# Kernel tuning notes

Measured on AMD Instinct MI355X. Metric: run time of the kernel, lower is better.

Reference implementation:

```python
import jax, jax.numpy as jnp
import numpy as np

B, N, M, D, H = 2, 2048, 2048, 1024, 16
HD = D // H          # head_dim = 64
F = int(D * 4.0)     # mlp hidden = 4096
EPS = 1e-5


def layernorm(x, w, b):
    mu = jnp.mean(x, axis=-1, keepdims=True)
    var = jnp.mean(jnp.square(x - mu), axis=-1, keepdims=True)
    return (x - mu) * jax.lax.rsqrt(var + EPS) * w + b


def setup_inputs() -> dict:
    key = jax.random.key(0)
    ks = jax.random.split(key, 8)
    w = lambda k, shape: jax.random.normal(k, shape, dtype=jnp.float32) * 0.02
    return {
        "query": jax.random.normal(ks[0], (B, N, D), dtype=jnp.float32),
        "context": jax.random.normal(ks[1], (B, M, D), dtype=jnp.float32),
        "qpos": jax.random.randint(ks[2], (B, N), 0, N, dtype=jnp.int32),
        "cpos": jax.random.randint(ks[3], (B, M), 0, M, dtype=jnp.int32),
        "Wq_w": w(ks[4], (D, D)), "Wq_b": jnp.zeros((D,), jnp.float32),
        "Wk_w": w(ks[5], (D, D)), "Wk_b": jnp.zeros((D,), jnp.float32),
        "Wv_w": w(ks[6], (D, D)), "Wv_b": jnp.zeros((D,), jnp.float32),
        "qn_w": jnp.ones((HD,), jnp.float32), "qn_b": jnp.zeros((HD,), jnp.float32),
        "kn_w": jnp.ones((HD,), jnp.float32), "kn_b": jnp.zeros((HD,), jnp.float32),
        "ffn_w": jnp.ones((D,), jnp.float32), "ffn_b": jnp.zeros((D,), jnp.float32),
        "fc1_w": w(ks[7], (D, F)), "fc1_b": jnp.zeros((F,), jnp.float32),
        "fc2_w": w(jax.random.fold_in(key, 99), (F, D)), "fc2_b": jnp.zeros((D,), jnp.float32),
    }


def reference(query, context, qpos, cpos,
              Wq_w, Wq_b, Wk_w, Wk_b, Wv_w, Wv_b,
              qn_w, qn_b, kn_w, kn_b,
              ffn_w, ffn_b, fc1_w, fc1_b, fc2_w, fc2_b):
    # rope=None -> qpos/cpos unused (kept for signature fidelity)
    res = query
    # QKV projections, split heads -> (B,H,T,HD)
    Q = (query @ Wq_w + Wq_b).reshape(B, N, H, HD).transpose(0, 2, 1, 3)
    K = (context @ Wk_w + Wk_b).reshape(B, M, H, HD).transpose(0, 2, 1, 3)
    V = (context @ Wv_w + Wv_b).reshape(B, M, H, HD).transpose(0, 2, 1, 3)
    # per-head LayerNorm on q and k
    Q = layernorm(Q, qn_w, qn_b)
    K = layernorm(K, kn_w, kn_b)
    # attention
    scores = jnp.einsum('bhnd,bhmd->bhnm', Q, K) / jnp.sqrt(jnp.float32(HD))
    attn = jax.nn.softmax(scores, axis=-1)
    out = jnp.einsum('bhnm,bhmd->bhnd', attn, V)
    out = out.transpose(0, 2, 1, 3).reshape(B, N, D)
    out = res + out
    # MLP block with pre-norm
    res2 = out
    h = layernorm(out, ffn_w, ffn_b)
    h = jax.nn.gelu(h @ fc1_w + fc1_b, approximate=False)
    h = h @ fc2_w + fc2_b
    return res2 + h
```

## Files before the change

### kernel.cpp

```cpp
#include <hip/hip_runtime.h>
#include <hip/hip_bf16.h>
#include <math.h>

constexpr int Bb  = 2;
constexpr int Nn  = 2048;
constexpr int Mm  = 2048;
constexpr int Dd  = 1024;
constexpr int Hh  = 16;
constexpr int HD  = 64;
constexpr int Ff  = 4096;
constexpr float EPS = 1e-5f;
constexpr float QSCALE = 0.125f * 1.4426950408889634f;
constexpr float SMAX = 12.0f;

typedef __attribute__((ext_vector_type(8))) short bf16x8;
typedef __attribute__((ext_vector_type(4))) short bf16x4;
typedef __attribute__((ext_vector_type(4))) float f32x4;

__device__ inline unsigned short f2bf(float f) {
    __hip_bfloat16 h = __float2bfloat16(f);
    return *reinterpret_cast<unsigned short*>(&h);
}
__device__ inline unsigned short f2bf_rh(float f) {
    union { float f; unsigned u; } c{f};
    return (unsigned short)((c.u + 0x8000u) >> 16);
}
__device__ inline float bf2f(unsigned short u) {
    union { unsigned u; float f; } c{(unsigned)u << 16};
    return c.f;
}

__device__ inline float gelu_fast(float x) {
    float t = x * x;
    float f = fmaf(-0.10295004f, t, -2.30211782f);
    float e = __builtin_amdgcn_exp2f(x * f);
    return x * __builtin_amdgcn_rcpf(1.0f + e);
}

__device__ inline void async_load16(const void* g, void* l) {
    __builtin_amdgcn_global_load_lds(
        (const __attribute__((address_space(1))) void*)g,
        (__attribute__((address_space(3))) void*)l, 16, 0, 0);
}

__global__ __launch_bounds__(256) void prep_kernel(
    const float* __restrict__ query, const float* __restrict__ context,
    unsigned short* __restrict__ qa, unsigned short* __restrict__ ca,
    const float* __restrict__ W0, const float* __restrict__ W1,
    const float* __restrict__ W2, const float* __restrict__ W3,
    const float* __restrict__ W4,
    unsigned short* __restrict__ T0, unsigned short* __restrict__ T1,
    unsigned short* __restrict__ T2, unsigned short* __restrict__ T3,
    unsigned short* __restrict__ T4)
{
    __shared__ float tile[32][33];
    int bid = blockIdx.x;
    if (bid < 8192) {
        int i = bid * 256 + threadIdx.x;
        const float* x; unsigned short* y; int k;
        if (i < 1048576) { x = query; y = qa; k = i; }
        else { x = context; y = ca; k = i - 1048576; }
        float4 v = reinterpret_cast<const float4*>(x)[k];
        ushort4 o;
        o.x = f2bf(v.x); o.y = f2bf(v.y); o.z = f2bf(v.z); o.w = f2bf(v.w);
        reinterpret_cast<ushort4*>(y)[k] = o;
        return;
    }
    bid -= 8192;
    const float* W; unsigned short* T; int K, Cn, tid;
    if (bid < 3072) {
        int j = bid >> 10; tid = bid & 1023;
        W = (j == 0) ? W0 : (j == 1) ? W1 : W2;
        T = (j == 0) ? T0 : (j == 1) ? T1 : T2;
        K = Dd; Cn = Dd;
    } else if (bid < 7168) {
        tid = bid - 3072; W = W3; T = T3; K = Dd; Cn = Ff;
    } else {
        tid = bid - 7168; W = W4; T = T4; K = Ff; Cn = Dd;
    }
    int xt = Cn >> 5;
    int bx = tid % xt, by = tid / xt;
    int tx = threadIdx.x & 31, ty = threadIdx.x >> 5;
    int c = bx * 32 + tx;
    int kbase = by * 32;
#pragma unroll
    for (int i = ty; i < 32; i += 8)
        tile[i][tx] = W[(size_t)(kbase + i) * Cn + c];
    __syncthreads();
    int k = kbase + tx;
#pragma unroll
    for (int i = ty; i < 32; i += 8)
        T[(size_t)(bx * 32 + i) * K + k] = f2bf(tile[tx][i]);
}

__global__ __launch_bounds__(256) void qkv_fused_kernel(
    const unsigned short* __restrict__ qa, const unsigned short* __restrict__ ca,
    const unsigned short* __restrict__ Wqt, const unsigned short* __restrict__ Wkt,
    const unsigned short* __restrict__ Wvt,
    const float* __restrict__ bq, const float* __restrict__ bk,
    const float* __restrict__ bv,
    const float* __restrict__ qn_w, const float* __restrict__ qn_b,
    const float* __restrict__ kn_w, const float* __restrict__ kn_b,
    unsigned short* __restrict__ Qbh, unsigned short* __restrict__ Kbh,
    unsigned short* __restrict__ Vt_g)
{
    __shared__ __align__(16) unsigned short As[2][128 * 32];
    __shared__ __align__(16) unsigned short Bs[2][128 * 32];

    const int bz = blockIdx.z;
    const unsigned short* A  = (bz == 0) ? qa : ca;
    const unsigned short* Bt = (bz == 0) ? Wqt : (bz == 1) ? Wkt : Wvt;
    const float* bias        = (bz == 0) ? bq  : (bz == 1) ? bk  : bv;
    const int K = Dd;

    const int t    = threadIdx.x;
    const int wave = t >> 6;
    const int lane = t & 63;
    const int r0 = blockIdx.y * 128;
    const int c0 = blockIdx.x * 128;
    const int wm = (wave >> 1) * 64;
    const int wn = (wave & 1) * 64;

    f32x4 acc[4][4];
#pragma unroll
    for (int i = 0; i < 4; i++)
#pragma unroll
        for (int j = 0; j < 4; j++) acc[i][j] = (f32x4)0.0f;

    const int row1 = t >> 2;
    const int kcs  = ((t & 3) ^ ((t >> 3) & 3)) * 8;
    const size_t arow1 = (size_t)(r0 + row1) * K + kcs;
    const size_t arow2 = (size_t)(r0 + row1 + 64) * K + kcs;
    const size_t brow1 = (size_t)(c0 + row1) * K + kcs;
    const size_t brow2 = (size_t)(c0 + row1 + 64) * K + kcs;
    char* A1_0 = (char*)&As[0][0] + wave * 1024;
    char* A2_0 = (char*)&As[0][0] + 4096 + wave * 1024;
    char* B1_0 = (char*)&Bs[0][0] + wave * 1024;
    char* B2_0 = (char*)&Bs[0][0] + 4096 + wave * 1024;
    char* A1_1 = (char*)&As[1][0] + wave * 1024;
    char* A2_1 = (char*)&As[1][0] + 4096 + wave * 1024;
    char* B1_1 = (char*)&Bs[1][0] + wave * 1024;
    char* B2_1 = (char*)&Bs[1][0] + 4096 + wave * 1024;

    const int m   = lane & 15;
    const int swc = ((lane >> 4) ^ ((m >> 1) & 3)) << 3;

    async_load16(A + arow1, A1_0);
    async_load16(A + arow2, A2_0);
    async_load16(Bt + brow1, B1_0);
    async_load16(Bt + brow2, B2_0);

    for (int k0 = 0; k0 < K; k0 += 32) {
        __syncthreads();
        const int cur = (k0 >> 5) & 1;
        if (k0 + 32 < K) {
            const int nk = k0 + 32;
            async_load16(A + arow1 + nk, cur ? A1_0 : A1_1);
            async_load16(A + arow2 + nk, cur ? A2_0 : A2_1);
            async_load16(Bt + brow1 + nk, cur ? B1_0 : B1_1);
            async_load16(Bt + brow2 + nk, cur ? B2_0 : B2_1);
        }
        const unsigned short* Ac = &As[cur][0];
        const unsigned short* Bc = &Bs[cur][0];

        bf16x8 af[4], bfr[4];
#pragma unroll
        for (int mi = 0; mi < 4; mi++)
            af[mi] = *(const bf16x8*)&Ac[(wm + mi * 16 + m) * 32 + swc];
#pragma unroll
        for (int nj = 0; nj < 4; nj++)
            bfr[nj] = *(const bf16x8*)&Bc[(wn + nj * 16 + m) * 32 + swc];
#pragma unroll
        for (int mi = 0; mi < 4; mi++)
#pragma unroll
            for (int nj = 0; nj < 4; nj++)
                acc[mi][nj] = __builtin_amdgcn_mfma_f32_16x16x32_bf16(
                    af[mi], bfr[nj], acc[mi][nj], 0, 0, 0);
    }

    const int rowb = r0 + wm + (lane >> 4) * 4;
    const int colb = c0 + wn + m;
#pragma unroll
    for (int nj = 0; nj < 4; nj++) {
        float bvv = bias[colb + nj * 16];
#pragma unroll
        for (int mi = 0; mi < 4; mi++)
#pragma unroll
            for (int r = 0; r < 4; r++) acc[mi][nj][r] += bvv;
    }

    if (bz < 2) {
        unsigned short* O = (bz == 0) ? Qbh : Kbh;
        const float* lw = (bz == 0) ? qn_w : kn_w;
        const float* lb = (bz == 0) ? qn_b : kn_b;
        const float scale = (bz == 0) ? QSCALE : 1.0f;
        const int hcol = c0 + wn;
        float w4[4], b4[4];
#pragma unroll
        for (int nj = 0; nj < 4; nj++) {
            int d = nj * 16 + m;
            w4[nj] = lw[d]; b4[nj] = lb[d];
        }
#pragma unroll
        for (int mi = 0; mi < 4; mi++) {
#pragma unroll
            for (int r = 0; r < 4; r++) {
                float s = (acc[mi][0][r] + acc[mi][1][r]) +
                          (acc[mi][2][r] + acc[mi][3][r]);
                s += __shfl_xor(s, 1); s += __shfl_xor(s, 2);
                s += __shfl_xor(s, 4); s += __shfl_xor(s, 8);
                float mu = s * (1.0f / 64.0f);
                float v2 = 0.f;
#pragma unroll
                for (int nj = 0; nj < 4; nj++) {
                    float dd = acc[mi][nj][r] - mu; v2 += dd * dd;
                }
                v2 += __shfl_xor(v2, 1); v2 += __shfl_xor(v2, 2);
                v2 += __shfl_xor(v2, 4); v2 += __shfl_xor(v2, 8);
                float rstd = rsqrtf(v2 * (1.0f / 64.0f) + EPS);
                size_t base = (size_t)(rowb + mi * 16 + r) * Dd + hcol;
#pragma unroll
                for (int nj = 0; nj < 4; nj++) {
                    int d = nj * 16 + m;
                    O[base + d] = f2bf(
                        ((acc[mi][nj][r] - mu) * rstd * w4[nj] + b4[nj]) * scale);
                }
            }
        }
    } else {
#pragma unroll
        for (int mi = 0; mi < 4; mi++) {
            int row0 = rowb + mi * 16;
            int bidx = row0 >> 11;
            int mtok = row0 & (Mm - 1);
#pragma unroll
            for (int nj = 0; nj < 4; nj++) {
                int col = colb + nj * 16;
                int h = col >> 6, d = col & 63;
                ushort4 o;
                o.x = f2bf(acc[mi][nj][0]);
                o.y = f2bf(acc[mi][nj][1]);
                o.z = f2bf(acc[mi][nj][2]);
                o.w = f2bf(acc[mi][nj][3]);
                *(ushort4*)(Vt_g + (((size_t)(bidx * Hh + h) * HD + d) << 11) + mtok) = o;
            }
        }
    }
}

#define QUAD(MH, BB, NH)                                                      \
    {                                                                         \
        _Pragma("unroll")                                                     \
        for (int miq = 0; miq < 4; ++miq) {                                   \
            _Pragma("unroll")                                                 \
            for (int njq = 0; njq < 2; ++njq) {                               \
                _Pragma("unroll")                                             \
                for (int ks = 0; ks < 2; ++ks) {                              \
                    acc[(MH) * 4 + miq][(NH) * 2 + njq] =                     \
                        __builtin_amdgcn_mfma_f32_16x16x32_bf16(              \
                            afr[miq][ks], BB[njq][ks],                        \
                            acc[(MH) * 4 + miq][(NH) * 2 + njq], 0, 0, 0);    \
                }                                                             \
            }                                                                 \
        }                                                                     \
    }

template <int MODE>
__global__ __launch_bounds__(512, 2) void gemm_8ph(
    const unsigned short* __restrict__ A,
    const unsigned short* __restrict__ Bt,
    const float* __restrict__ bias,
    unsigned short* __restrict__ Out)
{
    extern __shared__ char smem[];

    constexpr int KstC = (MODE == 0) ? Dd : Ff;
    constexpr int CnC  = (MODE == 0) ? Ff : Dd;
    constexpr int NI   = 16;

    const int chunk  = blockIdx.x & 7;
    const int within = blockIdx.x >> 3;
    int r0, c0, koff = 0;
    if (MODE == 0) {
        const int bx = (chunk & 3) * 4 + (within & 3);
        const int by = (chunk >> 2) * 8 + (within >> 2);
        r0 = by * 256; c0 = bx * 256;
    } else {
        const int split = chunk >> 1;
        const int bx = within & 3;
        const int by = (chunk & 1) * 8 + (within >> 2);
        r0 = by * 256; c0 = bx * 256; koff = split * (Ff / 4);
        Out += (size_t)split * ((size_t)Bb * Nn * Dd);
    }

    const int t    = threadIdx.x;
    const int wave = t >> 6;
    const int lane = t & 63;
    const int m16  = lane & 15;
    const int kg4  = lane >> 4;
    const int wr   = wave >> 2;
    const int wc   = wave & 3;

    const int u  = t >> 3;
    const int cl = ((t & 7) ^ (u & 7)) * 8;
    const unsigned short* sA0 = A + (size_t)(r0 + u) * KstC + koff + cl;
    const unsigned short* sA1 = A + (size_t)(r0 + 128 + u) * KstC + koff + cl;
    const int rB = (u & 31) + ((u >> 5) << 6);
    const unsigned short* sB0 = Bt + (size_t)(c0 + rB) * KstC + koff + cl;
    const unsigned short* sB1 = Bt + (size_t)(c0 + 128 + rB) * KstC + koff + cl;

    int rdA[4], rdB[2], ck[2];
#pragma unroll
    for (int miq = 0; miq < 4; miq++) rdA[miq] = (wr * 64 + miq * 16 + m16) * 128;
#pragma unroll
    for (int njq = 0; njq < 2; njq++) rdB[njq] = (wc * 32 + njq * 16 + m16) * 128;
#pragma unroll
    for (int ks = 0; ks < 2; ks++) ck[ks] = (((ks * 4 + kg4) ^ (m16 & 7)) << 4);

    f32x4 acc[8][4];
#pragma unroll
    for (int i = 0; i < 8; i++)
#pragma unroll
        for (int j = 0; j < 4; j++) acc[i][j] = (f32x4)0.0f;

    bf16x8 afr[4][2], b0r[2][2], b1r[2][2];

    auto stA = [&](int mh, int nd, int kel) {
        char* d = smem + nd * 65536 + mh * 16384 + wave * 1024;
        async_load16(sA0 + (size_t)mh * 64 * KstC + kel, d);
        async_load16(sA1 + (size_t)mh * 64 * KstC + kel, d + 8192);
    };
    auto stB = [&](int nh, int nd, int kel) {
        char* d = smem + nd * 65536 + 32768 + nh * 16384 + wave * 1024;
        async_load16(sB0 + (size_t)nh * 32 * KstC + kel, d);
        async_load16(sB1 + (size_t)nh * 32 * KstC + kel, d + 8192);
    };
    auto ldA = [&](int cd, int mh) {
        const char* base = smem + cd * 65536 + mh * 16384;
#pragma unroll
        for (int miq = 0; miq < 4; miq++)
#pragma unroll
            for (int ks = 0; ks < 2; ks++)
                afr[miq][ks] = *(const bf16x8*)(base + rdA[miq] + ck[ks]);
    };
    auto ldB = [&](int cd, int nh, bf16x8 (&bb)[2][2]) {
        const char* base = smem + cd * 65536 + 32768 + nh * 16384;
#pragma unroll
        for (int njq = 0; njq < 2; njq++)
#pragma unroll
            for (int ks = 0; ks < 2; ks++)
                bb[njq][ks] = *(const bf16x8*)(base + rdB[njq] + ck[ks]);
    };

    stA(0, 0, 0); stB(0, 0, 0); stB(1, 0, 0); stA(1, 0, 0);
    asm volatile("s_waitcnt vmcnt(0)" ::: "memory");
    asm volatile("s_barrier" ::: "memory");

    for (int it = 0; it < NI - 1; ++it) {
        const int cd = it & 1, nd = cd ^ 1;
        const int kn = (it + 1) * 64;
        ldA(cd, 0); ldB(cd, 0, b0r);
        stA(0, nd, kn);
        asm volatile("s_waitcnt vmcnt(4)" ::: "memory");
        asm volatile("s_barrier" ::: "memory");
        QUAD(0, b0r, 0)
        ldB(cd, 1, b1r);
        stB(0, nd, kn);
        asm volatile("s_waitcnt vmcnt(4)" ::: "memory");
        asm volatile("s_barrier" ::: "memory");
        QUAD(0, b1r, 1)
        ldA(cd, 1);
        stB(1, nd, kn);
        asm volatile("s_barrier" ::: "memory");
        QUAD(1, b1r, 1)
        stA(1, nd, kn);
        asm volatile("s_waitcnt vmcnt(4)" ::: "memory");
        asm volatile("s_barrier" ::: "memory");
        QUAD(1, b0r, 0)
    }

    {
        const int cd = (NI - 1) & 1;
        ldA(cd, 0); ldB(cd, 0, b0r);
        asm volatile("s_waitcnt vmcnt(2)" ::: "memory");
        asm volatile("s_barrier" ::: "memory");
        QUAD(0, b0r, 0)
        ldB(cd, 1, b1r);
        asm volatile("s_waitcnt vmcnt(0)" ::: "memory");
        asm volatile("s_barrier" ::: "memory");
        QUAD(0, b1r, 1)
        ldA(cd, 1);
        QUAD(1, b1r, 1)
        QUAD(1, b0r, 0)
    }

#pragma unroll
    for (int MI = 0; MI < 8; MI++) {
        const int row = r0 + wr * 128 + MI * 16 + kg4 * 4;
#pragma unroll
        for (int NJ = 0; NJ < 4; NJ++) {
            const int col = c0 + wc * 64 + NJ * 16 + m16;
            if (MODE == 0) {
                const float bv = bias[col];
#pragma unroll
                for (int rr = 0; rr < 4; rr++) {
                    float v = acc[MI][NJ][rr] + bv;
                    v = gelu_fast(v);
                    Out[(size_t)(row + rr) * CnC + col] = f2bf(v);
                }
            } else {
#pragma unroll
                for (int rr = 0; rr < 4; rr++)
                    Out[(size_t)(row + rr) * CnC + col] = f2bf(acc[MI][NJ][rr]);
            }
        }
    }
}

__global__ __launch_bounds__(512) void attention_mfma_kernel(
    const unsigned short* __restrict__ Qb,
    const unsigned short* __restrict__ Kb,
    const unsigned short* __restrict__ Vt_g,
    const float* __restrict__ query,
    float* __restrict__ Out);

namespace {
struct GemmAttrInit {
    GemmAttrInit() {
        hipFuncSetAttribute(reinterpret_cast<const void*>(&gemm_8ph<0>),
                            hipFuncAttributeMaxDynamicSharedMemorySize, 131072);
        hipFuncSetAttribute(reinterpret_cast<const void*>(&gemm_8ph<1>),
                            hipFuncAttributeMaxDynamicSharedMemorySize, 131072);
        hipFuncSetAttribute(reinterpret_cast<const void*>(&attention_mfma_kernel),
                            hipFuncAttributeMaxDynamicSharedMemorySize, 69632);
    }
};
GemmAttrInit g_gemm_attr_init;
}

__global__ __launch_bounds__(256) void fc2_reduce_kernel(
    const unsigned short* __restrict__ Part, const float* __restrict__ bias,
    const float* __restrict__ attn, float* __restrict__ out)
{
    constexpr size_t NEl = (size_t)Bb * Nn * Dd;
    size_t i4 = (size_t)blockIdx.x * 256 + threadIdx.x;
    size_t i = i4 * 4;
    float4 s = *reinterpret_cast<const float4*>(attn + i);
    float4 bv = *reinterpret_cast<const float4*>(bias + (i & (Dd - 1)));
    s.x += bv.x; s.y += bv.y; s.z += bv.z; s.w += bv.w;
#pragma unroll
    for (int sp = 0; sp < 4; sp++) {
        ushort4 u = *reinterpret_cast<const ushort4*>(Part + sp * NEl + i);
        s.x += bf2f(u.x); s.y += bf2f(u.y); s.z += bf2f(u.z); s.w += bf2f(u.w);
    }
    *reinterpret_cast<float4*>(out + i) = s;
}

__global__ __launch_bounds__(256) void ln_row_bf16_kernel(
    const float* __restrict__ X, const float* __restrict__ w,
    const float* __restrict__ b, unsigned short* __restrict__ Y)
{
    int row = blockIdx.x;
    const float* x = X + (size_t)row * Dd;
    int t = threadIdx.x;
    float v[4];
    float s = 0.f;
#pragma unroll
    for (int i = 0; i < 4; i++) { v[i] = x[t + i * 256]; s += v[i]; }
#pragma unroll
    for (int off = 32; off; off >>= 1) s += __shfl_xor(s, off);
    __shared__ float red[4];
    __shared__ float stats[2];
    if ((t & 63) == 0) red[t >> 6] = s;
    __syncthreads();
    if (t == 0) stats[0] = (red[0] + red[1] + red[2] + red[3]) * (1.0f / Dd);
    __syncthreads();
    float mu = stats[0];
    float s2 = 0.f;
#pragma unroll
    for (int i = 0; i < 4; i++) { float d = v[i] - mu; s2 += d * d; }
#pragma unroll
    for (int off = 32; off; off >>= 1) s2 += __shfl_xor(s2, off);
    __syncthreads();
    if ((t & 63) == 0) red[t >> 6] = s2;
    __syncthreads();
    if (t == 0) stats[1] = (red[0] + red[1] + red[2] + red[3]) * (1.0f / Dd);
    __syncthreads();
    float rstd = rsqrtf(stats[1] + EPS);
    unsigned short* y = Y + (size_t)row * Dd;
#pragma unroll
    for (int i = 0; i < 4; i++) {
        int c = t + i * 256;
        y[c] = f2bf((v[i] - mu) * rstd * w[c] + b[c]);
    }
}

__global__ __launch_bounds__(512) void attention_mfma_kernel(
    const unsigned short* __restrict__ Qb,
    const unsigned short* __restrict__ Kb,
    const unsigned short* __restrict__ Vt_g,
    const float* __restrict__ query,
    float* __restrict__ Out)
{
    extern __shared__ char asmem[];

    const int bid = blockIdx.x;
    const int g  = bid & 31;
    const int qt = bid >> 5;
    const int b  = g >> 4;
    const int h  = g & 15;
    const int q0 = qt * 256;

    const int t    = threadIdx.x;
    const int wave = t >> 6;
    const int lane = t & 63;
    const int m16  = lane & 15;
    const int kg   = lane >> 4;
    const int swc  = (kg ^ ((m16 >> 1) & 3)) << 3;

    bf16x8 qf[2][2];
#pragma unroll
    for (int rh = 0; rh < 2; rh++) {
        const unsigned short* qp =
            Qb + ((size_t)(b * Nn + q0 + wave * 32 + rh * 16 + m16) * Dd + h * HD + kg * 8);
        qf[rh][0] = *(const bf16x8*)qp;
        qf[rh][1] = *(const bf16x8*)(qp + 32);
    }

    f32x4 oacc[2][4];
    float lrow[2][4];
#pragma unroll
    for (int rh = 0; rh < 2; rh++)
#pragma unroll
        for (int i = 0; i < 4; i++) { oacc[rh][i] = (f32x4)0.f; lrow[rh][i] = 0.f; }

    const size_t kbase  = (size_t)(b * Mm) * Dd + h * HD;
    const size_t vtbase = ((size_t)(b * Hh + h) * HD) * Mm;
    unsigned short* psw = (unsigned short*)(asmem + 32768) + wave * (32 * 72);

    const int u    = t & 255;
    const int pan  = t >> 8;
    const int srow = u >> 2;
    const int schk = ((u & 3) ^ ((srow >> 1) & 3)) * 8;
    char* kdstA = asmem +     0 + pan * 4096 + (wave & 3) * 1024;
    char* kdstB = asmem +  8192 + pan * 4096 + (wave & 3) * 1024;
    char* vdstA = asmem + 16384 + pan * 4096 + (wave & 3) * 1024;
    char* vdstB = asmem + 24576 + pan * 4096 + (wave & 3) * 1024;
    const unsigned short* kp0 = Kb + kbase + (size_t)srow * Dd + schk + pan * 32;
    const unsigned short* vp0 = Vt_g + vtbase + (size_t)srow * Mm + schk + pan * 32;

    async_load16(kp0, kdstA);
    async_load16(vp0, vdstA);

    for (int m0 = 0; m0 < Mm; m0 += 64) {
        __syncthreads();
        const int cur = (m0 >> 6) & 1;
        if (m0 + 64 < Mm) {
            async_load16(kp0 + (size_t)(m0 + 64) * Dd, cur ? kdstA : kdstB);
            async_load16(vp0 + (m0 + 64),              cur ? vdstA : vdstB);
        }
        const unsigned short* Kc = (const unsigned short*)(asmem + cur * 8192);
        const unsigned short* Vc = (const unsigned short*)(asmem + 16384 + cur * 8192);

        f32x4 s[2][4];
#pragma unroll
        for (int j = 0; j < 4; j++) {
            bf16x8 b0 = *(const bf16x8*)&Kc[(j * 16 + m16) * 32 + swc];
            bf16x8 b1 = *(const bf16x8*)&Kc[2048 + (j * 16 + m16) * 32 + swc];
#pragma unroll
            for (int rh = 0; rh < 2; rh++) {
                f32x4 a = (f32x4)(-SMAX);
                a = __builtin_amdgcn_mfma_f32_16x16x32_bf16(qf[rh][0], b0, a, 0, 0, 0);
                a = __builtin_amdgcn_mfma_f32_16x16x32_bf16(qf[rh][1], b1, a, 0, 0, 0);
                s[rh][j] = a;
            }
        }

#pragma unroll
        for (int rh = 0; rh < 2; rh++) {
#pragma unroll
            for (int r = 0; r < 4; r++) {
                float p0 = __builtin_amdgcn_exp2f(s[rh][0][r]);
                float p1 = __builtin_amdgcn_exp2f(s[rh][1][r]);
                float p2 = __builtin_amdgcn_exp2f(s[rh][2][r]);
                float p3 = __builtin_amdgcn_exp2f(s[rh][3][r]);
                lrow[rh][r] += (p0 + p1) + (p2 + p3);
                int qrow = rh * 16 + kg * 4 + r;
                psw[qrow * 72 +  0 + m16] = f2bf_rh(p0);
                psw[qrow * 72 + 16 + m16] = f2bf_rh(p1);
                psw[qrow * 72 + 32 + m16] = f2bf_rh(p2);
                psw[qrow * 72 + 48 + m16] = f2bf_rh(p3);
            }
        }

        bf16x8 pf[2][2];
#pragma unroll
        for (int rh = 0; rh < 2; rh++) {
            pf[rh][0] = *(const bf16x8*)(psw + (rh * 16 + m16) * 72 + kg * 8);
            pf[rh][1] = *(const bf16x8*)(psw + (rh * 16 + m16) * 72 + 32 + kg * 8);
        }
#pragma unroll
        for (int dj = 0; dj < 4; dj++) {
            bf16x8 v0 = *(const bf16x8*)&Vc[(dj * 16 + m16) * 32 + swc];
            bf16x8 v1 = *(const bf16x8*)&Vc[2048 + (dj * 16 + m16) * 32 + swc];
#pragma unroll
            for (int rh = 0; rh < 2; rh++) {
                oacc[rh][dj] = __builtin_amdgcn_mfma_f32_16x16x32_bf16(pf[rh][0], v0, oacc[rh][dj], 0, 0, 0);
                oacc[rh][dj] = __builtin_amdgcn_mfma_f32_16x16x32_bf16(pf[rh][1], v1, oacc[rh][dj], 0, 0, 0);
            }
        }
    }

#pragma unroll
    for (int rh = 0; rh < 2; rh++) {
#pragma unroll
        for (int r = 0; r < 4; r++) {
            float l = lrow[rh][r];
            l += __shfl_xor(l, 1);
            l += __shfl_xor(l, 2);
            l += __shfl_xor(l, 4);
            l += __shfl_xor(l, 8);
            float inv = 1.0f / l;
            const size_t rowbase =
                (size_t)(b * Nn + q0 + wave * 32 + rh * 16 + kg * 4 + r) * Dd + h * HD;
#pragma unroll
            for (int dj = 0; dj < 4; dj++) {
                size_t idx = rowbase + dj * 16 + m16;
                Out[idx] = query[idx] + oacc[rh][dj][r] * inv;
            }
        }
    }
}

extern "C" void kernel_launch(void* const* d_in, const int* in_sizes, int n_in,
                              void* d_out, int out_size, void* d_ws, size_t ws_size,
                              hipStream_t stream)
{
    const float* query   = (const float*)d_in[0];
    const float* context = (const float*)d_in[1];
    const float* Wq_w = (const float*)d_in[4];
    const float* Wq_b = (const float*)d_in[5];
    const float* Wk_w = (const float*)d_in[6];
    const float* Wk_b = (const float*)d_in[7];
    const float* Wv_w = (const float*)d_in[8];
    const float* Wv_b = (const float*)d_in[9];
    const float* qn_w = (const float*)d_in[10];
    const float* qn_b = (const float*)d_in[11];
    const float* kn_w = (const float*)d_in[12];
    const float* kn_b = (const float*)d_in[13];
    const float* ffn_w = (const float*)d_in[14];
    const float* ffn_b = (const float*)d_in[15];
    const float* fc1_w = (const float*)d_in[16];
    const float* fc1_b = (const float*)d_in[17];
    const float* fc2_w = (const float*)d_in[18];
    const float* fc2_b = (const float*)d_in[19];

    constexpr size_t BND = (size_t)Bb * Nn * Dd;
    constexpr size_t BMD = (size_t)Bb * Mm * Dd;
    constexpr size_t DD  = (size_t)Dd * Dd;
    constexpr size_t DF  = (size_t)Dd * Ff;

    static bool attr_done = false;
    if (!attr_done) {
        hipFuncSetAttribute(reinterpret_cast<const void*>(&gemm_8ph<0>),
                            hipFuncAttributeMaxDynamicSharedMemorySize, 131072);
        hipFuncSetAttribute(reinterpret_cast<const void*>(&gemm_8ph<1>),
                            hipFuncAttributeMaxDynamicSharedMemorySize, 131072);
        hipFuncSetAttribute(reinterpret_cast<const void*>(&attention_mfma_kernel),
                            hipFuncAttributeMaxDynamicSharedMemorySize, 69632);
        attr_done = true;
    }

    const size_t need = BND * 4 + (2 * BND + 3 * BMD) * 2 + (3 * DD + 2 * DF) * 2
                      + 4 * BND * 2;
    if (ws_size < need) return;

    char* p = (char*)d_ws;
    float* attn = (float*)p;                   p += BND * 4;
    unsigned short* Qbh  = (unsigned short*)p; p += BND * 2;
    unsigned short* Kbh  = (unsigned short*)p; p += BMD * 2;
    unsigned short* Vt_g = (unsigned short*)p; p += BMD * 2;
    unsigned short* qa   = (unsigned short*)p; p += BND * 2;
    unsigned short* ca   = (unsigned short*)p; p += BMD * 2;
    unsigned short* Wqt  = (unsigned short*)p; p += DD * 2;
    unsigned short* Wkt  = (unsigned short*)p; p += DD * 2;
    unsigned short* Wvt  = (unsigned short*)p; p += DD * 2;
    unsigned short* fc1t = (unsigned short*)p; p += DF * 2;
    unsigned short* fc2t = (unsigned short*)p; p += DF * 2;
    unsigned short* part = (unsigned short*)p; p += 4 * BND * 2;
    unsigned short* normed = Qbh;
    unsigned short* mid    = Kbh;
    float* out = (float*)d_out;

    const int R = Bb * Nn;
    dim3 blk(256);

    prep_kernel<<<19456, blk, 0, stream>>>(
        query, context, qa, ca,
        Wq_w, Wk_w, Wv_w, fc1_w, fc2_w, Wqt, Wkt, Wvt, fc1t, fc2t);

    qkv_fused_kernel<<<dim3(Dd / 128, R / 128, 3), blk, 0, stream>>>(
        qa, ca, Wqt, Wkt, Wvt, Wq_b, Wk_b, Wv_b,
        qn_w, qn_b, kn_w, kn_b, Qbh, Kbh, Vt_g);

    attention_mfma_kernel<<<Bb * Hh * (Nn / 256), 512, 69632, stream>>>(
        Qbh, Kbh, Vt_g, query, attn);

    ln_row_bf16_kernel<<<Bb * Nn, blk, 0, stream>>>(attn, ffn_w, ffn_b, normed);

    gemm_8ph<0><<<256, 512, 131072, stream>>>(normed, fc1t, fc1_b, mid);
    gemm_8ph<1><<<256, 512, 131072, stream>>>(mid, fc2t, nullptr, part);
    fc2_reduce_kernel<<<BND / 4 / 256, blk, 0, stream>>>(
        part, fc2_b, attn, out);
}
```

Measured before the change: 334.1 us.

## Replace QKV projection kernel with 256x256-tile 8-phase pipelined GEMM

The QKV projection kernel, which used 128x128 tiles with double-buffered 32-wide K steps, is replaced by a new qkv_8ph kernel. It reuses the tuned gemm_8ph main loop, factored into a shared macro: 256x256 tiles, 512 threads, 64-wide K steps, 128 KB of dynamic LDS, and interleaved async loads and barriers. The per-head LayerNorm, bias and V-transpose epilogue is kept. The aim is better data reuse and MFMA throughput. The cost is only 192 blocks in the grid, with a chunked block order chosen for L2 locality, so GPU occupancy may suffer.

New measurement: 321.6 us. 3.7% less time.

```diff
diff --git a/kernel.cpp b/kernel.cpp
--- a/kernel.cpp
+++ b/kernel.cpp
@@ -93,161 +93,6 @@
         T[(size_t)(bx * 32 + i) * K + k] = f2bf(tile[tx][i]);
 }
 
-__global__ __launch_bounds__(256) void qkv_fused_kernel(
-    const unsigned short* __restrict__ qa, const unsigned short* __restrict__ ca,
-    const unsigned short* __restrict__ Wqt, const unsigned short* __restrict__ Wkt,
-    const unsigned short* __restrict__ Wvt,
-    const float* __restrict__ bq, const float* __restrict__ bk,
-    const float* __restrict__ bv,
-    const float* __restrict__ qn_w, const float* __restrict__ qn_b,
-    const float* __restrict__ kn_w, const float* __restrict__ kn_b,
-    unsigned short* __restrict__ Qbh, unsigned short* __restrict__ Kbh,
-    unsigned short* __restrict__ Vt_g)
-{
-    __shared__ __align__(16) unsigned short As[2][128 * 32];
-    __shared__ __align__(16) unsigned short Bs[2][128 * 32];
-
-    const int bz = blockIdx.z;
-    const unsigned short* A  = (bz == 0) ? qa : ca;
-    const unsigned short* Bt = (bz == 0) ? Wqt : (bz == 1) ? Wkt : Wvt;
-    const float* bias        = (bz == 0) ? bq  : (bz == 1) ? bk  : bv;
-    const int K = Dd;
-
-    const int t    = threadIdx.x;
-    const int wave = t >> 6;
-    const int lane = t & 63;
-    const int r0 = blockIdx.y * 128;
-    const int c0 = blockIdx.x * 128;
-    const int wm = (wave >> 1) * 64;
-    const int wn = (wave & 1) * 64;
-
-    f32x4 acc[4][4];
-#pragma unroll
-    for (int i = 0; i < 4; i++)
-#pragma unroll
-        for (int j = 0; j < 4; j++) acc[i][j] = (f32x4)0.0f;
-
-    const int row1 = t >> 2;
-    const int kcs  = ((t & 3) ^ ((t >> 3) & 3)) * 8;
-    const size_t arow1 = (size_t)(r0 + row1) * K + kcs;
-    const size_t arow2 = (size_t)(r0 + row1 + 64) * K + kcs;
-    const size_t brow1 = (size_t)(c0 + row1) * K + kcs;
-    const size_t brow2 = (size_t)(c0 + row1 + 64) * K + kcs;
-    char* A1_0 = (char*)&As[0][0] + wave * 1024;
-    char* A2_0 = (char*)&As[0][0] + 4096 + wave * 1024;
-    char* B1_0 = (char*)&Bs[0][0] + wave * 1024;
-    char* B2_0 = (char*)&Bs[0][0] + 4096 + wave * 1024;
-    char* A1_1 = (char*)&As[1][0] + wave * 1024;
-    char* A2_1 = (char*)&As[1][0] + 4096 + wave * 1024;
-    char* B1_1 = (char*)&Bs[1][0] + wave * 1024;
-    char* B2_1 = (char*)&Bs[1][0] + 4096 + wave * 1024;
-
-    const int m   = lane & 15;
-    const int swc = ((lane >> 4) ^ ((m >> 1) & 3)) << 3;
-
-    async_load16(A + arow1, A1_0);
-    async_load16(A + arow2, A2_0);
-    async_load16(Bt + brow1, B1_0);
-    async_load16(Bt + brow2, B2_0);
-
-    for (int k0 = 0; k0 < K; k0 += 32) {
-        __syncthreads();
-        const int cur = (k0 >> 5) & 1;
-        if (k0 + 32 < K) {
-            const int nk = k0 + 32;
-            async_load16(A + arow1 + nk, cur ? A1_0 : A1_1);
-            async_load16(A + arow2 + nk, cur ? A2_0 : A2_1);
-            async_load16(Bt + brow1 + nk, cur ? B1_0 : B1_1);
-            async_load16(Bt + brow2 + nk, cur ? B2_0 : B2_1);
-        }
-        const unsigned short* Ac = &As[cur][0];
-        const unsigned short* Bc = &Bs[cur][0];
-
-        bf16x8 af[4], bfr[4];
-#pragma unroll
-        for (int mi = 0; mi < 4; mi++)
-            af[mi] = *(const bf16x8*)&Ac[(wm + mi * 16 + m) * 32 + swc];
-#pragma unroll
-        for (int nj = 0; nj < 4; nj++)
-            bfr[nj] = *(const bf16x8*)&Bc[(wn + nj * 16 + m) * 32 + swc];
-#pragma unroll
-        for (int mi = 0; mi < 4; mi++)
-#pragma unroll
-            for (int nj = 0; nj < 4; nj++)
-                acc[mi][nj] = __builtin_amdgcn_mfma_f32_16x16x32_bf16(
-                    af[mi], bfr[nj], acc[mi][nj], 0, 0, 0);
-    }
-
-    const int rowb = r0 + wm + (lane >> 4) * 4;
-    const int colb = c0 + wn + m;
-#pragma unroll
-    for (int nj = 0; nj < 4; nj++) {
-        float bvv = bias[colb + nj * 16];
-#pragma unroll
-        for (int mi = 0; mi < 4; mi++)
-#pragma unroll
-            for (int r = 0; r < 4; r++) acc[mi][nj][r] += bvv;
-    }
-
-    if (bz < 2) {
-        unsigned short* O = (bz == 0) ? Qbh : Kbh;
-        const float* lw = (bz == 0) ? qn_w : kn_w;
-        const float* lb = (bz == 0) ? qn_b : kn_b;
-        const float scale = (bz == 0) ? QSCALE : 1.0f;
-        const int hcol = c0 + wn;
-        float w4[4], b4[4];
-#pragma unroll
-        for (int nj = 0; nj < 4; nj++) {
-            int d = nj * 16 + m;
-            w4[nj] = lw[d]; b4[nj] = lb[d];
-        }
-#pragma unroll
-        for (int mi = 0; mi < 4; mi++) {
-#pragma unroll
-            for (int r = 0; r < 4; r++) {
-                float s = (acc[mi][0][r] + acc[mi][1][r]) +
-                          (acc[mi][2][r] + acc[mi][3][r]);
-                s += __shfl_xor(s, 1); s += __shfl_xor(s, 2);
-                s += __shfl_xor(s, 4); s += __shfl_xor(s, 8);
-                float mu = s * (1.0f / 64.0f);
-                float v2 = 0.f;
-#pragma unroll
-                for (int nj = 0; nj < 4; nj++) {
-                    float dd = acc[mi][nj][r] - mu; v2 += dd * dd;
-                }
-                v2 += __shfl_xor(v2, 1); v2 += __shfl_xor(v2, 2);
-                v2 += __shfl_xor(v2, 4); v2 += __shfl_xor(v2, 8);
-                float rstd = rsqrtf(v2 * (1.0f / 64.0f) + EPS);
-                size_t base = (size_t)(rowb + mi * 16 + r) * Dd + hcol;
-#pragma unroll
-                for (int nj = 0; nj < 4; nj++) {
-                    int d = nj * 16 + m;
-                    O[base + d] = f2bf(
-                        ((acc[mi][nj][r] - mu) * rstd * w4[nj] + b4[nj]) * scale);
-                }
-            }
-        }
-    } else {
-#pragma unroll
-        for (int mi = 0; mi < 4; mi++) {
-            int row0 = rowb + mi * 16;
-            int bidx = row0 >> 11;
-            int mtok = row0 & (Mm - 1);
-#pragma unroll
-            for (int nj = 0; nj < 4; nj++) {
-                int col = colb + nj * 16;
-                int h = col >> 6, d = col & 63;
-                ushort4 o;
-                o.x = f2bf(acc[mi][nj][0]);
-                o.y = f2bf(acc[mi][nj][1]);
-                o.z = f2bf(acc[mi][nj][2]);
-                o.w = f2bf(acc[mi][nj][3]);
-                *(ushort4*)(Vt_g + (((size_t)(bidx * Hh + h) * HD + d) << 11) + mtok) = o;
-            }
-        }
-    }
-}
-
 #define QUAD(MH, BB, NH)                                                      \
     {                                                                         \
         _Pragma("unroll")                                                     \
@@ -265,6 +110,47 @@
         }                                                                     \
     }
 
+#define GEMM8PH_MAIN(NI)                                                      \
+    stA(0, 0, 0); stB(0, 0, 0); stB(1, 0, 0); stA(1, 0, 0);                   \
+    asm volatile("s_waitcnt vmcnt(0)" ::: "memory");                          \
+    asm volatile("s_barrier" ::: "memory");                                   \
+    for (int it = 0; it < (NI) - 1; ++it) {                                   \
+        const int cd = it & 1, nd = cd ^ 1;                                   \
+        const int kn = (it + 1) * 64;                                         \
+        ldA(cd, 0); ldB(cd, 0, b0r);                                          \
+        stA(0, nd, kn);                                                       \
+        asm volatile("s_waitcnt vmcnt(4)" ::: "memory");                      \
+        asm volatile("s_barrier" ::: "memory");                               \
+        QUAD(0, b0r, 0)                                                       \
+        ldB(cd, 1, b1r);                                                      \
+        stB(0, nd, kn);                                                       \
+        asm volatile("s_waitcnt vmcnt(4)" ::: "memory");                      \
+        asm volatile("s_barrier" ::: "memory");                               \
+        QUAD(0, b1r, 1)                                                       \
+        ldA(cd, 1);                                                           \
+        stB(1, nd, kn);                                                       \
+        asm volatile("s_barrier" ::: "memory");                               \
+        QUAD(1, b1r, 1)                                                       \
+        stA(1, nd, kn);                                                       \
+        asm volatile("s_waitcnt vmcnt(4)" ::: "memory");                      \
+        asm volatile("s_barrier" ::: "memory");                               \
+        QUAD(1, b0r, 0)                                                       \
+    }                                                                         \
+    {                                                                         \
+        const int cd = ((NI) - 1) & 1;                                        \
+        ldA(cd, 0); ldB(cd, 0, b0r);                                          \
+        asm volatile("s_waitcnt vmcnt(2)" ::: "memory");                      \
+        asm volatile("s_barrier" ::: "memory");                               \
+        QUAD(0, b0r, 0)                                                       \
+        ldB(cd, 1, b1r);                                                      \
+        asm volatile("s_waitcnt vmcnt(0)" ::: "memory");                      \
+        asm volatile("s_barrier" ::: "memory");                               \
+        QUAD(0, b1r, 1)                                                       \
+        ldA(cd, 1);                                                           \
+        QUAD(1, b1r, 1)                                                       \
+        QUAD(1, b0r, 0)                                                       \
+    }
+
 template <int MODE>
 __global__ __launch_bounds__(512, 2) void gemm_8ph(
     const unsigned short* __restrict__ A,
@@ -352,47 +238,7 @@
                 bb[njq][ks] = *(const bf16x8*)(base + rdB[njq] + ck[ks]);
     };
 
-    stA(0, 0, 0); stB(0, 0, 0); stB(1, 0, 0); stA(1, 0, 0);
-    asm volatile("s_waitcnt vmcnt(0)" ::: "memory");
-    asm volatile("s_barrier" ::: "memory");
-
-    for (int it = 0; it < NI - 1; ++it) {
-        const int cd = it & 1, nd = cd ^ 1;
-        const int kn = (it + 1) * 64;
-        ldA(cd, 0); ldB(cd, 0, b0r);
-        stA(0, nd, kn);
-        asm volatile("s_waitcnt vmcnt(4)" ::: "memory");
-        asm volatile("s_barrier" ::: "memory");
-        QUAD(0, b0r, 0)
-        ldB(cd, 1, b1r);
-        stB(0, nd, kn);
-        asm volatile("s_waitcnt vmcnt(4)" ::: "memory");
-        asm volatile("s_barrier" ::: "memory");
-        QUAD(0, b1r, 1)
-        ldA(cd, 1);
-        stB(1, nd, kn);
-        asm volatile("s_barrier" ::: "memory");
-        QUAD(1, b1r, 1)
-        stA(1, nd, kn);
-        asm volatile("s_waitcnt vmcnt(4)" ::: "memory");
-        asm volatile("s_barrier" ::: "memory");
-        QUAD(1, b0r, 0)
-    }
-
-    {
-        const int cd = (NI - 1) & 1;
-        ldA(cd, 0); ldB(cd, 0, b0r);
-        asm volatile("s_waitcnt vmcnt(2)" ::: "memory");
-        asm volatile("s_barrier" ::: "memory");
-        QUAD(0, b0r, 0)
-        ldB(cd, 1, b1r);
-        asm volatile("s_waitcnt vmcnt(0)" ::: "memory");
-        asm volatile("s_barrier" ::: "memory");
-        QUAD(0, b1r, 1)
-        ldA(cd, 1);
-        QUAD(1, b1r, 1)
-        QUAD(1, b0r, 0)
-    }
+    GEMM8PH_MAIN(NI)
 
 #pragma unroll
     for (int MI = 0; MI < 8; MI++) {
@@ -417,6 +263,164 @@
     }
 }
 
+__global__ __launch_bounds__(512, 2) void qkv_8ph(
+    const unsigned short* __restrict__ qa, const unsigned short* __restrict__ ca,
+    const unsigned short* __restrict__ Wqt, const unsigned short* __restrict__ Wkt,
+    const unsigned short* __restrict__ Wvt,
+    const float* __restrict__ bq, const float* __restrict__ bk,
+    const float* __restrict__ bv,
+    const float* __restrict__ qn_w, const float* __restrict__ qn_b,
+    const float* __restrict__ kn_w, const float* __restrict__ kn_b,
+    unsigned short* __restrict__ Qbh, unsigned short* __restrict__ Kbh,
+    unsigned short* __restrict__ Vt_g)
+{
+    extern __shared__ char smem[];
+
+    constexpr int KstC = Dd;
+    constexpr int NI   = 16;
+
+    const int chunk  = blockIdx.x & 7;
+    const int within = blockIdx.x >> 3;
+    const int bz     = within >> 3;
+    const int t8     = within & 7;
+    const int by     = chunk * 2 + (t8 >> 2);
+    const int bx     = t8 & 3;
+    const int r0 = by * 256, c0 = bx * 256;
+
+    const unsigned short* A  = (bz == 0) ? qa : ca;
+    const unsigned short* Bt = (bz == 0) ? Wqt : (bz == 1) ? Wkt : Wvt;
+    const float* bias        = (bz == 0) ? bq  : (bz == 1) ? bk  : bv;
+
+    const int t    = threadIdx.x;
+    const int wave = t >> 6;
+    const int lane = t & 63;
+    const int m16  = lane & 15;
+    const int kg4  = lane >> 4;
+    const int wr   = wave >> 2;
+    const int wc   = wave & 3;
+
+    const int u  = t >> 3;
+    const int cl = ((t & 7) ^ (u & 7)) * 8;
+    const unsigned short* sA0 = A + (size_t)(r0 + u) * KstC + cl;
+    const unsigned short* sA1 = A + (size_t)(r0 + 128 + u) * KstC + cl;
+    const int rB = (u & 31) + ((u >> 5) << 6);
+    const unsigned short* sB0 = Bt + (size_t)(c0 + rB) * KstC + cl;
+    const unsigned short* sB1 = Bt + (size_t)(c0 + 128 + rB) * KstC + cl;
+
+    int rdA[4], rdB[2], ck[2];
+#pragma unroll
+    for (int miq = 0; miq < 4; miq++) rdA[miq] = (wr * 64 + miq * 16 + m16) * 128;
+#pragma unroll
+    for (int njq = 0; njq < 2; njq++) rdB[njq] = (wc * 32 + njq * 16 + m16) * 128;
+#pragma unroll
+    for (int ks = 0; ks < 2; ks++) ck[ks] = (((ks * 4 + kg4) ^ (m16 & 7)) << 4);
+
+    f32x4 acc[8][4];
+#pragma unroll
+    for (int i = 0; i < 8; i++)
+#pragma unroll
+        for (int j = 0; j < 4; j++) acc[i][j] = (f32x4)0.0f;
+
+    bf16x8 afr[4][2], b0r[2][2], b1r[2][2];
+
+    auto stA = [&](int mh, int nd, int kel) {
+        char* d = smem + nd * 65536 + mh * 16384 + wave * 1024;
+        async_load16(sA0 + (size_t)mh * 64 * KstC + kel, d);
+        async_load16(sA1 + (size_t)mh * 64 * KstC + kel, d + 8192);
+    };
+    auto stB = [&](int nh, int nd, int kel) {
+        char* d = smem + nd * 65536 + 32768 + nh * 16384 + wave * 1024;
+        async_load16(sB0 + (size_t)nh * 32 * KstC + kel, d);
+        async_load16(sB1 + (size_t)nh * 32 * KstC + kel, d + 8192);
+    };
+    auto ldA = [&](int cd, int mh) {
+        const char* base = smem + cd * 65536 + mh * 16384;
+#pragma unroll
+        for (int miq = 0; miq < 4; miq++)
+#pragma unroll
+            for (int ks = 0; ks < 2; ks++)
+                afr[miq][ks] = *(const bf16x8*)(base + rdA[miq] + ck[ks]);
+    };
+    auto ldB = [&](int cd, int nh, bf16x8 (&bb)[2][2]) {
+        const char* base = smem + cd * 65536 + 32768 + nh * 16384;
+#pragma unroll
+        for (int njq = 0; njq < 2; njq++)
+#pragma unroll
+            for (int ks = 0; ks < 2; ks++)
+                bb[njq][ks] = *(const bf16x8*)(base + rdB[njq] + ck[ks]);
+    };
+
+    GEMM8PH_MAIN(NI)
+
+#pragma unroll
+    for (int NJ = 0; NJ < 4; NJ++) {
+        float bvv = bias[c0 + wc * 64 + NJ * 16 + m16];
+#pragma unroll
+        for (int MI = 0; MI < 8; MI++)
+#pragma unroll
+            for (int r = 0; r < 4; r++) acc[MI][NJ][r] += bvv;
+    }
+
+    if (bz < 2) {
+        unsigned short* O = (bz == 0) ? Qbh : Kbh;
+        const float* lw = (bz == 0) ? qn_w : kn_w;
+        const float* lb = (bz == 0) ? qn_b : kn_b;
+        const float scale = (bz == 0) ? QSCALE : 1.0f;
+        const int hcol = c0 + wc * 64;
+        float w4[4], b4[4];
+#pragma unroll
+        for (int NJ = 0; NJ < 4; NJ++) {
+            int d = NJ * 16 + m16;
+            w4[NJ] = lw[d]; b4[NJ] = lb[d];
+        }
+#pragma unroll
+        for (int MI = 0; MI < 8; MI++) {
+#pragma unroll
+            for (int r = 0; r < 4; r++) {
+                float s = (acc[MI][0][r] + acc[MI][1][r]) +
+                          (acc[MI][2][r] + acc[MI][3][r]);
+                s += __shfl_xor(s, 1); s += __shfl_xor(s, 2);
+                s += __shfl_xor(s, 4); s += __shfl_xor(s, 8);
+                float mu = s * (1.0f / 64.0f);
+                float v2 = 0.f;
+#pragma unroll
+                for (int NJ = 0; NJ < 4; NJ++) {
+                    float dd = acc[MI][NJ][r] - mu; v2 += dd * dd;
+                }
+                v2 += __shfl_xor(v2, 1); v2 += __shfl_xor(v2, 2);
+                v2 += __shfl_xor(v2, 4); v2 += __shfl_xor(v2, 8);
+                float rstd = rsqrtf(v2 * (1.0f / 64.0f) + EPS);
+                const int row = r0 + wr * 128 + MI * 16 + kg4 * 4 + r;
+                size_t base = (size_t)row * Dd + hcol;
+#pragma unroll
+                for (int NJ = 0; NJ < 4; NJ++) {
+                    int d = NJ * 16 + m16;
+                    O[base + d] = f2bf(
+                        ((acc[MI][NJ][r] - mu) * rstd * w4[NJ] + b4[NJ]) * scale);
+                }
+            }
+        }
+    } else {
+#pragma unroll
+        for (int MI = 0; MI < 8; MI++) {
+            const int row0 = r0 + wr * 128 + MI * 16 + kg4 * 4;
+            const int bidx = row0 >> 11;
+            const int mtok = row0 & (Mm - 1);
+#pragma unroll
+            for (int NJ = 0; NJ < 4; NJ++) {
+                const int col = c0 + wc * 64 + NJ * 16 + m16;
+                const int h = col >> 6, d = col & 63;
+                ushort4 o;
+                o.x = f2bf(acc[MI][NJ][0]);
+                o.y = f2bf(acc[MI][NJ][1]);
+                o.z = f2bf(acc[MI][NJ][2]);
+                o.w = f2bf(acc[MI][NJ][3]);
+                *(ushort4*)(Vt_g + (((size_t)(bidx * Hh + h) * HD + d) << 11) + mtok) = o;
+            }
+        }
+    }
+}
+
 __global__ __launch_bounds__(512) void attention_mfma_kernel(
     const unsigned short* __restrict__ Qb,
     const unsigned short* __restrict__ Kb,
@@ -430,6 +434,8 @@
         hipFuncSetAttribute(reinterpret_cast<const void*>(&gemm_8ph<0>),
                             hipFuncAttributeMaxDynamicSharedMemorySize, 131072);
         hipFuncSetAttribute(reinterpret_cast<const void*>(&gemm_8ph<1>),
+                            hipFuncAttributeMaxDynamicSharedMemorySize, 131072);
+        hipFuncSetAttribute(reinterpret_cast<const void*>(&qkv_8ph),
                             hipFuncAttributeMaxDynamicSharedMemorySize, 131072);
         hipFuncSetAttribute(reinterpret_cast<const void*>(&attention_mfma_kernel),
                             hipFuncAttributeMaxDynamicSharedMemorySize, 69632);
@@ -666,6 +672,8 @@
                             hipFuncAttributeMaxDynamicSharedMemorySize, 131072);
         hipFuncSetAttribute(reinterpret_cast<const void*>(&gemm_8ph<1>),
                             hipFuncAttributeMaxDynamicSharedMemorySize, 131072);
+        hipFuncSetAttribute(reinterpret_cast<const void*>(&qkv_8ph),
+                            hipFuncAttributeMaxDynamicSharedMemorySize, 131072);
         hipFuncSetAttribute(reinterpret_cast<const void*>(&attention_mfma_kernel),
                             hipFuncAttributeMaxDynamicSharedMemorySize, 69632);
         attr_done = true;
@@ -692,14 +700,13 @@
     unsigned short* mid    = Kbh;
     float* out = (float*)d_out;
 
-    const int R = Bb * Nn;
     dim3 blk(256);
 
     prep_kernel<<<19456, blk, 0, stream>>>(
         query, context, qa, ca,
         Wq_w, Wk_w, Wv_w, fc1_w, fc2_w, Wqt, Wkt, Wvt, fc1t, fc2t);
 
-    qkv_fused_kernel<<<dim3(Dd / 128, R / 128, 3), blk, 0, stream>>>(
+    qkv_8ph<<<192, 512, 131072, stream>>>(
         qa, ca, Wqt, Wkt, Wvt, Wq_b, Wk_b, Wv_b,
         qn_w, qn_b, kn_w, kn_b, Qbh, Kbh, Vt_g);
 
```
